# Kernel tuning notes

Measured on AMD Instinct MI355X. Metric: run time of the kernel, lower is better.

The kernel has to match this reference:

```python
import jax, jax.numpy as jnp
import numpy as np

V, C, T, H, L, B = 32000, 1024, 1024, 16, 8, 4
HS = C // H
STD = 0.02


def _layernorm(x, g, b, eps=1e-5):
    m = jnp.mean(x, axis=-1, keepdims=True)
    v = jnp.mean(jnp.square(x - m), axis=-1, keepdims=True)
    return (x - m) * jax.lax.rsqrt(v + eps) * g + b


def setup_inputs() -> dict:
    key = jax.random.key(0)
    ks = jax.random.split(key, 16)
    n = lambda k, shape: (jax.random.normal(k, shape, dtype=jnp.float32) * STD)
    return {
        "index": jax.random.randint(ks[0], (B, T), 0, V),
        "targets": jax.random.randint(ks[1], (B, T), 0, V),
        "tok_emb": n(ks[2], (V, C)),
        "pos_emb": n(ks[3], (T, C)),
        "wq": n(ks[4], (L, C, C)),
        "wk": n(ks[5], (L, C, C)),
        "wv": n(ks[6], (L, C, C)),
        "wo": n(ks[7], (L, C, C)),
        "bo": jnp.zeros((L, C), jnp.float32),
        "w1": n(ks[8], (L, C, 4 * C)),
        "b1": jnp.zeros((L, 4 * C), jnp.float32),
        "w2": n(ks[9], (L, 4 * C, C)),
        "b2": jnp.zeros((L, C), jnp.float32),
        "ln1_g": jnp.ones((L, C), jnp.float32),
        "ln1_b": jnp.zeros((L, C), jnp.float32),
        "ln2_g": jnp.ones((L, C), jnp.float32),
        "ln2_b": jnp.zeros((L, C), jnp.float32),
        "lnf_g": jnp.ones((C,), jnp.float32),
        "lnf_b": jnp.zeros((C,), jnp.float32),
        "lm_w": n(ks[10], (C, V)),
        "lm_b": jnp.zeros((V,), jnp.float32),
    }


def reference(index, targets, tok_emb, pos_emb, wq, wk, wv, wo, bo, w1, b1, w2,
              b2, ln1_g, ln1_b, ln2_g, ln2_b, lnf_g, lnf_b, lm_w, lm_b):
    b, t = index.shape
    x = tok_emb[index] + pos_emb[:t]                      # [B,T,C]
    causal = jnp.tril(jnp.ones((t, t), dtype=bool))       # tril mask
    scale = HS ** -0.5
    for l in range(L):  # fixed small layer loop
        q = (x @ wq[l]).reshape(b, t, H, HS)
        k = (x @ wk[l]).reshape(b, t, H, HS)
        v = (x @ wv[l]).reshape(b, t, H, HS)
        scores = jnp.einsum('bqhd,bkhd->bhqk', q, k) * scale
        scores = jnp.where(causal, scores, -jnp.inf)
        w = jax.nn.softmax(scores, axis=-1)               # dropout p=0 -> identity
        att = jnp.einsum('bhqk,bkhd->bqhd', w, v).reshape(b, t, C)
        x = _layernorm(x + att @ wo[l] + bo[l], ln1_g[l], ln1_b[l])
        h = jax.nn.relu(x @ w1[l] + b1[l])
        x = _layernorm(x + h @ w2[l] + b2[l], ln2_g[l], ln2_b[l])
    x = _layernorm(x, lnf_g, lnf_b)
    logits = (x @ lm_w + lm_b).reshape(b * t, V)
    logp = jax.nn.log_softmax(logits, axis=-1)
    loss = -jnp.take_along_axis(logp, targets.reshape(-1, 1), axis=1).mean()
    return logits, loss
```

## Files before the change

kernel.cpp:

```cpp
#include <hip/hip_runtime.h>

typedef unsigned short u16;
typedef __attribute__((ext_vector_type(4))) float f32x4;
typedef __attribute__((ext_vector_type(8))) short s16x8;
typedef __attribute__((ext_vector_type(4))) short s16x4;

static constexpr int V = 32000;
static constexpr int C = 1024;
static constexpr int T = 1024;
static constexpr int H = 16;
static constexpr int L = 8;
static constexpr int B = 4;
static constexpr int HS = 64;
static constexpr int BT = B * T;
static constexpr int C4 = 4 * C;
static constexpr int C3 = 3 * C;

__device__ __forceinline__ u16 f2bf(float f) {
  union { float f; unsigned u; } v; v.f = f;
  unsigned r = v.u + 0x7fffu + ((v.u >> 16) & 1u);
  return (u16)(r >> 16);
}

__device__ __forceinline__ void gload16(const u16* g, u16* l) {
  __builtin_amdgcn_global_load_lds(
      (const __attribute__((address_space(1))) void*)g,
      (__attribute__((address_space(3))) void*)l, 16, 0, 0);
}

__device__ __forceinline__ float blockReduceSum(float v) {
  __shared__ float red[4];
  int lane = threadIdx.x & 63, w = threadIdx.x >> 6;
#pragma unroll
  for (int m = 32; m >= 1; m >>= 1) v += __shfl_xor(v, m, 64);
  if (lane == 0) red[w] = v;
  __syncthreads();
  float r = red[0] + red[1] + red[2] + red[3];
  __syncthreads();
  return r;
}

__global__ __launch_bounds__(256) void k_embed(
    const int* __restrict__ idx, const float* __restrict__ tok,
    const float* __restrict__ pos, float* __restrict__ x, u16* __restrict__ xb) {
  int bt = blockIdx.x;
  int t = bt & (T - 1);
  int row = idx[bt];
  int tid = threadIdx.x;
  f32x4 tv = ((const f32x4*)(tok + (size_t)row * C))[tid];
  f32x4 pv = ((const f32x4*)(pos + (size_t)t * C))[tid];
  f32x4 y;
  s16x4 yb;
#pragma unroll
  for (int j = 0; j < 4; ++j) {
    y[j] = tv[j] + pv[j];
    yb[j] = (short)f2bf(y[j]);
  }
  ((f32x4*)(x + (size_t)bt * C))[tid] = y;
  ((s16x4*)(xb + (size_t)bt * C))[tid] = yb;
}

__global__ __launch_bounds__(256) void k_transpose(
    const float* __restrict__ W, u16* __restrict__ Wt, int K, int N,
    size_t sW, size_t sWt) {
  __shared__ float tile[64][65];
  const float* Wz = W + sW * blockIdx.z;
  u16* Wtz = Wt + sWt * blockIdx.z;
  int n0 = blockIdx.x * 64, k0 = blockIdx.y * 64;
  int tc = threadIdx.x & 63, tr = threadIdx.x >> 6;
#pragma unroll
  for (int i = 0; i < 16; ++i) {
    int r = tr + i * 4;
    tile[r][tc] = Wz[(size_t)(k0 + r) * N + (n0 + tc)];
  }
  __syncthreads();
#pragma unroll
  for (int i = 0; i < 16; ++i) {
    int r = tr + i * 4;
    Wtz[(size_t)(n0 + r) * K + (k0 + tc)] = f2bf(tile[tc][r]);
  }
}

template <int OUT_BF16, int RELU, int HAS_BIAS, int HAS_RES>
__global__ __launch_bounds__(256, 2) void k_gemm(
    const u16* __restrict__ A, const u16* __restrict__ Bt,
    const float* __restrict__ bias, const float* __restrict__ Res,
    float* __restrict__ Cf, u16* __restrict__ Cb, int M, int N, int K) {
  __shared__ u16 As[3][4096];
  __shared__ u16 Bs[3][4096];
  int tid = threadIdx.x;
  int lane = tid & 63, wid = tid >> 6;
  int lm = lane & 15, lg = lane >> 4;
  int wm = wid >> 1, wn = wid & 1;

  unsigned nbx = gridDim.x;
  unsigned nwg = nbx * gridDim.y;
  unsigned orig = blockIdx.y * nbx + blockIdx.x;
  unsigned f = ((nwg & 7u) == 0u) ? (orig & 7u) * (nwg >> 3) + (orig >> 3) : orig;
  int mb = (int)(f / nbx) * 128, nb = (int)(f % nbx) * 128;

  f32x4 acc[4][4];
#pragma unroll
  for (int i = 0; i < 4; ++i)
#pragma unroll
    for (int j = 0; j < 4; ++j) acc[i][j] = f32x4{0.f, 0.f, 0.f, 0.f};

  int r0 = tid >> 2, q0 = tid & 3;
  int r1 = (256 + tid) >> 2;
  const u16* a0 = A + (size_t)(mb + r0) * K + q0 * 8;
  const u16* a1 = A + (size_t)(mb + r1) * K + q0 * 8;
  const u16* b0 = Bt + (size_t)(nb + r0) * K + q0 * 8;
  const u16* b1 = Bt + (size_t)(nb + r1) * K + q0 * 8;
  const int ld0 = wid * 512, ld1 = 2048 + wid * 512;

  auto stage = [&](int t, int s) {
    int ko = t * 32;
    gload16(a0 + ko, &As[s][ld0]);
    gload16(a1 + ko, &As[s][ld1]);
    gload16(b0 + ko, &Bs[s][ld0]);
    gload16(b1 + ko, &Bs[s][ld1]);
  };

  int nK = K >> 5;
  stage(0, 0);
  stage(1, 1);
  for (int t = 0; t < nK; ++t) {
    int s = t % 3;
    if (t + 1 < nK)
      asm volatile("s_waitcnt vmcnt(4)" ::: "memory");
    else
      asm volatile("s_waitcnt vmcnt(0)" ::: "memory");
    __builtin_amdgcn_s_barrier();
    s16x8 af[4], bfr[4];
#pragma unroll
    for (int m = 0; m < 4; ++m)
      af[m] = *(const s16x8*)&As[s][(wm * 64 + m * 16 + lm) * 32 + lg * 8];
#pragma unroll
    for (int n = 0; n < 4; ++n)
      bfr[n] = *(const s16x8*)&Bs[s][(wn * 64 + n * 16 + lm) * 32 + lg * 8];
    if (t + 2 < nK) stage(t + 2, (t + 2) % 3);
    __builtin_amdgcn_s_setprio(1);
#pragma unroll
    for (int m = 0; m < 4; ++m)
#pragma unroll
      for (int n = 0; n < 4; ++n)
        acc[m][n] = __builtin_amdgcn_mfma_f32_16x16x32_bf16(af[m], bfr[n],
                                                            acc[m][n], 0, 0, 0);
    __builtin_amdgcn_s_setprio(0);
  }
#pragma unroll
  for (int m = 0; m < 4; ++m) {
#pragma unroll
    for (int n = 0; n < 4; ++n) {
      int col = nb + wn * 64 + n * 16 + lm;
      float bv = HAS_BIAS ? bias[col] : 0.0f;
#pragma unroll
      for (int r = 0; r < 4; ++r) {
        int row = mb + wm * 64 + m * 16 + lg * 4 + r;
        float v = acc[m][n][r] + bv;
        if (HAS_RES) v += Res[(size_t)row * N + col];
        if (RELU) v = v > 0.f ? v : 0.f;
        if (OUT_BF16)
          Cb[(size_t)row * N + col] = f2bf(v);
        else
          Cf[(size_t)row * N + col] = v;
      }
    }
  }
}

template <int OUT_BF16, int RELU, int HAS_BIAS, int HAS_RES, int VT>
__global__ __launch_bounds__(512) void k_gemm256(
    const u16* __restrict__ A, const u16* __restrict__ Bt,
    const float* __restrict__ bias, const float* __restrict__ Res,
    float* __restrict__ Cf, u16* __restrict__ Cb, u16* __restrict__ Vtp,
    int M, int N, int K) {
  __shared__ u16 As[2][16384];
  __shared__ u16 Bs[2][16384];
  const int tid = threadIdx.x;
  const int lane = tid & 63, wid = tid >> 6;
  const int lm = lane & 15, lg = lane >> 4;
  const int wr = wid >> 2, wc = wid & 3;

  unsigned nbx = gridDim.x;
  unsigned nwg = nbx * gridDim.y;
  unsigned orig = blockIdx.y * nbx + blockIdx.x;
  unsigned f =
      ((nwg & 7u) == 0u) ? (orig & 7u) * (nwg >> 3) + (orig >> 3) : orig;
  const int mb = (int)(f / nbx) * 256;
  const int nb = (int)(f % nbx) * 256;

  int aoff[4], boff[4], ldso[4];
#pragma unroll
  for (int h = 0; h < 4; ++h) {
    const int kk = h >> 1, p = h & 1;
    int rem = p * 512 + tid;
    int rblk = rem >> 6;
    int rem2 = rem & 63;
    int row16 = rem2 >> 2, psl = rem2 & 3;
    int sl = psl ^ ((row16 >> 1) & 3);
    int grow = rblk * 16 + row16;
    int gk = kk * 32 + sl * 8;
    aoff[h] = (mb + grow) * K + gk;
    boff[h] = (nb + grow) * K + gk;
    ldso[h] = kk * 8192 + p * 4096 + wid * 512;
  }
  const int lo = lm * 32 + ((lg ^ ((lm >> 1) & 3)) << 3);

  f32x4 acc[8][4];
#pragma unroll
  for (int i = 0; i < 8; ++i)
#pragma unroll
    for (int j = 0; j < 4; ++j) acc[i][j] = f32x4{0.f, 0.f, 0.f, 0.f};

  const int nK = K >> 6;
  gload16(A + aoff[0], &As[0][ldso[0]]);
  gload16(A + aoff[1], &As[0][ldso[1]]);
  gload16(Bt + boff[0], &Bs[0][ldso[0]]);
  gload16(Bt + boff[1], &Bs[0][ldso[1]]);
  gload16(A + aoff[2], &As[0][ldso[2]]);
  gload16(A + aoff[3], &As[0][ldso[3]]);
  gload16(Bt + boff[2], &Bs[0][ldso[2]]);
  gload16(Bt + boff[3], &Bs[0][ldso[3]]);
  asm volatile("s_waitcnt vmcnt(4)" ::: "memory");
  __builtin_amdgcn_s_barrier();

  for (int t = 0; t < nK; ++t) {
    const int buf = t & 1, nbuf = buf ^ 1;
    const bool pre = (t + 1 < nK);
    const int nk64 = (t + 1) * 64;
    s16x8 af[4], bfr[4];
#pragma unroll
    for (int m = 0; m < 4; ++m)
      af[m] = *(const s16x8*)&As[buf][(wr * 8 + m) * 512 + lo];
#pragma unroll
    for (int n = 0; n < 4; ++n)
      bfr[n] = *(const s16x8*)&Bs[buf][(wc * 4 + n) * 512 + lo];
    if (pre) {
      gload16(A + aoff[0] + nk64, &As[nbuf][ldso[0]]);
      gload16(A + aoff[1] + nk64, &As[nbuf][ldso[1]]);
    }
    __builtin_amdgcn_s_barrier();
    __builtin_amdgcn_s_setprio(1);
#pragma unroll
    for (int m = 0; m < 4; ++m)
#pragma unroll
      for (int n = 0; n < 4; ++n)
        acc[m][n] = __builtin_amdgcn_mfma_f32_16x16x32_bf16(af[m], bfr[n],
                                                            acc[m][n], 0, 0, 0);
    __builtin_amdgcn_s_setprio(0);
    __builtin_amdgcn_s_barrier();
#pragma unroll
    for (int m = 0; m < 4; ++m)
      af[m] = *(const s16x8*)&As[buf][(wr * 8 + 4 + m) * 512 + lo];
    if (pre) {
      gload16(Bt + boff[0] + nk64, &Bs[nbuf][ldso[0]]);
      gload16(Bt + boff[1] + nk64, &Bs[nbuf][ldso[1]]);
    }
    __builtin_amdgcn_s_barrier();
    __builtin_amdgcn_s_setprio(1);
#pragma unroll
    for (int m = 0; m < 4; ++m)
#pragma unroll
      for (int n = 0; n < 4; ++n)
        acc[m + 4][n] = __builtin_amdgcn_mfma_f32_16x16x32_bf16(
            af[m], bfr[n], acc[m + 4][n], 0, 0, 0);
    __builtin_amdgcn_s_setprio(0);
    __builtin_amdgcn_s_barrier();
#pragma unroll
    for (int m = 0; m < 4; ++m)
      af[m] = *(const s16x8*)&As[buf][8192 + (wr * 8 + m) * 512 + lo];
#pragma unroll
    for (int n = 0; n < 4; ++n)
      bfr[n] = *(const s16x8*)&Bs[buf][8192 + (wc * 4 + n) * 512 + lo];
    if (pre) {
      gload16(A + aoff[2] + nk64, &As[nbuf][ldso[2]]);
      gload16(A + aoff[3] + nk64, &As[nbuf][ldso[3]]);
      asm volatile("s_waitcnt vmcnt(6)" ::: "memory");
    } else {
      asm volatile("s_waitcnt vmcnt(0)" ::: "memory");
    }
    __builtin_amdgcn_s_barrier();
    __builtin_amdgcn_s_setprio(1);
#pragma unroll
    for (int m = 0; m < 4; ++m)
#pragma unroll
      for (int n = 0; n < 4; ++n)
        acc[m][n] = __builtin_amdgcn_mfma_f32_16x16x32_bf16(af[m], bfr[n],
                                                            acc[m][n], 0, 0, 0);
    __builtin_amdgcn_s_setprio(0);
    __builtin_amdgcn_s_barrier();
#pragma unroll
    for (int m = 0; m < 4; ++m)
      af[m] = *(const s16x8*)&As[buf][8192 + (wr * 8 + 4 + m) * 512 + lo];
    if (pre) {
      gload16(Bt + boff[2] + nk64, &Bs[nbuf][ldso[2]]);
      gload16(Bt + boff[3] + nk64, &Bs[nbuf][ldso[3]]);
      asm volatile("s_waitcnt vmcnt(4)" ::: "memory");
    }
    __builtin_amdgcn_s_barrier();
    __builtin_amdgcn_s_setprio(1);
#pragma unroll
    for (int m = 0; m < 4; ++m)
#pragma unroll
      for (int n = 0; n < 4; ++n)
        acc[m + 4][n] = __builtin_amdgcn_mfma_f32_16x16x32_bf16(
            af[m], bfr[n], acc[m + 4][n], 0, 0, 0);
    __builtin_amdgcn_s_setprio(0);
    __builtin_amdgcn_s_barrier();
  }
  if (VT && nb >= 2 * C) {
    int hh = ((nb - 2 * C) >> 6) + wc;
#pragma unroll
    for (int m = 0; m < 8; ++m) {
      int t0 = mb + wr * 128 + m * 16 + lg * 4;
      int bb = t0 >> 10, tt = t0 & (T - 1);
      size_t vbase = ((size_t)(bb * H + hh) * HS) * T + tt;
#pragma unroll
      for (int n = 0; n < 4; ++n) {
        int d = n * 16 + lm;
        s16x4 pk;
#pragma unroll
        for (int r = 0; r < 4; ++r) pk[r] = (short)f2bf(acc[m][n][r]);
        *(s16x4*)&Vtp[vbase + (size_t)d * T] = pk;
      }
    }
    return;
  }
  float bv[4];
#pragma unroll
  for (int n = 0; n < 4; ++n)
    bv[n] = HAS_BIAS ? bias[nb + wc * 64 + n * 16 + lm] : 0.0f;
#pragma unroll
  for (int m = 0; m < 8; ++m) {
#pragma unroll
    for (int r = 0; r < 4; ++r) {
      int row = mb + wr * 128 + m * 16 + lg * 4 + r;
#pragma unroll
      for (int n = 0; n < 4; ++n) {
        int col = nb + wc * 64 + n * 16 + lm;
        float v = acc[m][n][r] + bv[n];
        if (HAS_RES) v += Res[(size_t)row * N + col];
        if (RELU) v = v > 0.f ? v : 0.f;
        if (OUT_BF16)
          Cb[(size_t)row * N + col] = f2bf(v);
        else
          Cf[(size_t)row * N + col] = v;
      }
    }
  }
}

__global__ __launch_bounds__(512) void k_lmhead(
    const u16* __restrict__ A, const u16* __restrict__ Bt,
    const float* __restrict__ bias, float* __restrict__ Cf,
    float* __restrict__ Pp, int M, int N, int K) {
  __shared__ u16 As[3][4096];
  __shared__ u16 Bs[3][8192];
  const int tid = threadIdx.x;
  const int lane = tid & 63, wid = tid >> 6;
  const int lm = lane & 15, lg = lane >> 4;
  const int wr = wid >> 2, wc = wid & 3;

  unsigned nbx = gridDim.x;
  unsigned My = gridDim.y;
  unsigned nwg = nbx * My;
  unsigned orig = blockIdx.y * nbx + blockIdx.x;
  unsigned xcd = orig & 7u, idx = orig >> 3;
  unsigned g = xcd * (nwg >> 3) + idx;
  const int mb = (int)(g % My) * 128;
  const int nb = (int)(g / My) * 256;

  int rr0 = tid & 63;
  int row160 = rr0 >> 2, psl0 = rr0 & 3;
  int sl0 = psl0 ^ ((row160 >> 1) & 3);
  const int aoff = (mb + (tid >> 6) * 16 + row160) * K + sl0 * 8;
  const int lda = wid * 512;
  int boff[2], ldb[2];
#pragma unroll
  for (int p = 0; p < 2; ++p) {
    int rem = p * 512 + tid;
    int rblk = rem >> 6, rr = rem & 63;
    int row16 = rr >> 2, psl = rr & 3;
    int sl = psl ^ ((row16 >> 1) & 3);
    boff[p] = (nb + rblk * 16 + row16) * K + sl * 8;
    ldb[p] = p * 4096 + wid * 512;
  }
  const int lo = lm * 32 + ((lg ^ ((lm >> 1) & 3)) << 3);

  f32x4 acc[4][4];
#pragma unroll
  for (int i = 0; i < 4; ++i)
#pragma unroll
    for (int j = 0; j < 4; ++j) acc[i][j] = f32x4{0.f, 0.f, 0.f, 0.f};

  auto stage = [&](int t, int s) {
    int ko = t * 32;
    gload16(A + aoff + ko, &As[s][lda]);
    gload16(Bt + boff[0] + ko, &Bs[s][ldb[0]]);
    gload16(Bt + boff[1] + ko, &Bs[s][ldb[1]]);
  };

  const int nK = K >> 5;
  stage(0, 0);
  stage(1, 1);
  for (int t = 0; t < nK; ++t) {
    int s = t % 3;
    if (t + 1 < nK)
      asm volatile("s_waitcnt vmcnt(3)" ::: "memory");
    else
      asm volatile("s_waitcnt vmcnt(0)" ::: "memory");
    __builtin_amdgcn_s_barrier();
    s16x8 af[4], bfr[4];
#pragma unroll
    for (int m = 0; m < 4; ++m)
      af[m] = *(const s16x8*)&As[s][(wr * 4 + m) * 512 + lo];
#pragma unroll
    for (int n = 0; n < 4; ++n)
      bfr[n] = *(const s16x8*)&Bs[s][(wc * 4 + n) * 512 + lo];
    if (t + 2 < nK) stage(t + 2, (t + 2) % 3);
    __builtin_amdgcn_s_setprio(1);
#pragma unroll
    for (int m = 0; m < 4; ++m)
#pragma unroll
      for (int n = 0; n < 4; ++n)
        acc[m][n] = __builtin_amdgcn_mfma_f32_16x16x32_bf16(af[m], bfr[n],
                                                            acc[m][n], 0, 0, 0);
    __builtin_amdgcn_s_setprio(0);
  }
  float bv[4];
#pragma unroll
  for (int n = 0; n < 4; ++n) bv[n] = bias[nb + wc * 64 + n * 16 + lm];
#pragma unroll
  for (int m = 0; m < 4; ++m) {
#pragma unroll
    for (int r = 0; r < 4; ++r) {
      int row = mb + wr * 64 + m * 16 + lg * 4 + r;
#pragma unroll
      for (int n = 0; n < 4; ++n) {
        int col = nb + wc * 64 + n * 16 + lm;
        Cf[(size_t)row * N + col] = acc[m][n][r] + bv[n];
      }
    }
  }
  __syncthreads();
  float* redS = (float*)&As[0][0];
  float Sx[4][4];
#pragma unroll
  for (int m = 0; m < 4; ++m)
#pragma unroll
    for (int r = 0; r < 4; ++r)
      Sx[m][r] = __expf(acc[m][0][r] + bv[0]) + __expf(acc[m][1][r] + bv[1]) +
                 __expf(acc[m][2][r] + bv[2]) + __expf(acc[m][3][r] + bv[3]);
#pragma unroll
  for (int d = 1; d < 16; d <<= 1)
#pragma unroll
    for (int m = 0; m < 4; ++m)
#pragma unroll
      for (int r = 0; r < 4; ++r) Sx[m][r] += __shfl_xor(Sx[m][r], d, 16);
  if (lm == 0) {
#pragma unroll
    for (int m = 0; m < 4; ++m)
#pragma unroll
      for (int r = 0; r < 4; ++r)
        redS[(wr * 64 + m * 16 + lg * 4 + r) * 4 + wc] = Sx[m][r];
  }
  __syncthreads();
  if (tid < 128) {
    float srow = redS[tid * 4 + 0] + redS[tid * 4 + 1] + redS[tid * 4 + 2] +
                 redS[tid * 4 + 3];
    Pp[(size_t)(nb >> 8) * M + mb + tid] = srow;
  }
}

__global__ __launch_bounds__(256) void k_attn(
    const u16* __restrict__ qkv, const u16* __restrict__ vt,
    u16* __restrict__ o) {
  constexpr int PP = 72;
  __shared__ u16 Ks[2][64 * 64];
  __shared__ u16 Vs[2][64 * 64];
  __shared__ u16 Ps[4][16 * PP];
  int bid = blockIdx.x;
  int p = bid & 7, h = (bid >> 3) & 15, b = bid >> 7;
  int tid = threadIdx.x, lane = tid & 63, wid = tid >> 6;
  int lm = lane & 15, lg = lane >> 4;
  const size_t rowbase = (size_t)b * T * C3 + (size_t)h * HS;
  const u16* kbase = qkv + rowbase + C;
  const u16* vbase = vt + (size_t)(b * H + h) * HS * T;
  const size_t obase = (size_t)b * T * C + (size_t)h * HS;
  const float scale = 0.125f;
  const int sr = tid >> 3, scs = (tid & 7) ^ (sr & 7);
  const int swz0 = (lg ^ (lm & 7)) * 8;
  const int swz1 = ((4 + lg) ^ (lm & 7)) * 8;

  for (int qi = 0; qi < 2; ++qi) {
    int qt = qi ? (15 - p) : p;
    int qw = qt * 64 + wid * 16;
    s16x8 qf[2];
#pragma unroll
    for (int s = 0; s < 2; ++s)
      qf[s] = *(const s16x8*)&qkv[rowbase + (size_t)(qw + lm) * C3 + s * 32 +
                                  lg * 8];
    float m_[4], l_[4];
    f32x4 oacc[4];
#pragma unroll
    for (int r = 0; r < 4; ++r) { m_[r] = -3e38f; l_[r] = 0.f; }
#pragma unroll
    for (int n = 0; n < 4; ++n) oacc[n] = f32x4{0.f, 0.f, 0.f, 0.f};

    gload16(kbase + (size_t)sr * C3 + scs * 8, &Ks[0][wid * 512]);
    gload16(kbase + (size_t)(sr + 32) * C3 + scs * 8, &Ks[0][2048 + wid * 512]);
    gload16(vbase + (size_t)sr * T + scs * 8, &Vs[0][wid * 512]);
    gload16(vbase + (size_t)(sr + 32) * T + scs * 8, &Vs[0][2048 + wid * 512]);

    for (int kt = 0; kt <= qt; ++kt) {
      int buf = kt & 1;
      bool pre = kt < qt;
      if (pre) {
        int nk = (kt + 1) * 64;
        int nbuf = buf ^ 1;
        gload16(kbase + (size_t)(nk + sr) * C3 + scs * 8, &Ks[nbuf][wid * 512]);
        gload16(kbase + (size_t)(nk + sr + 32) * C3 + scs * 8,
                &Ks[nbuf][2048 + wid * 512]);
        gload16(vbase + (size_t)sr * T + nk + scs * 8, &Vs[nbuf][wid * 512]);
        gload16(vbase + (size_t)(sr + 32) * T + nk + scs * 8,
                &Vs[nbuf][2048 + wid * 512]);
        asm volatile("s_waitcnt vmcnt(4)" ::: "memory");
      } else {
        asm volatile("s_waitcnt vmcnt(0)" ::: "memory");
      }
      __builtin_amdgcn_s_barrier();

      f32x4 s[4];
#pragma unroll
      for (int ch = 0; ch < 4; ++ch) {
        s16x8 k0 = *(const s16x8*)&Ks[buf][(ch * 16 + lm) * 64 + swz0];
        s16x8 k1 = *(const s16x8*)&Ks[buf][(ch * 16 + lm) * 64 + swz1];
        s[ch] = f32x4{0.f, 0.f, 0.f, 0.f};
        s[ch] = __builtin_amdgcn_mfma_f32_16x16x32_bf16(qf[0], k0, s[ch], 0, 0, 0);
        s[ch] = __builtin_amdgcn_mfma_f32_16x16x32_bf16(qf[1], k1, s[ch], 0, 0, 0);
      }
      if (kt == qt) {
#pragma unroll
        for (int ch = 0; ch < 4; ++ch) {
          int col = kt * 64 + ch * 16 + lm;
#pragma unroll
          for (int r = 0; r < 4; ++r) {
            int row = qw + lg * 4 + r;
            s[ch][r] = (col <= row) ? s[ch][r] * scale : -3e38f;
          }
        }
      } else {
#pragma unroll
        for (int ch = 0; ch < 4; ++ch)
#pragma unroll
          for (int r = 0; r < 4; ++r) s[ch][r] *= scale;
      }
      float rmax[4];
#pragma unroll
      for (int r = 0; r < 4; ++r)
        rmax[r] = fmaxf(fmaxf(s[0][r], s[1][r]), fmaxf(s[2][r], s[3][r]));
#pragma unroll
      for (int mm = 1; mm < 16; mm <<= 1)
#pragma unroll
        for (int r = 0; r < 4; ++r)
          rmax[r] = fmaxf(rmax[r], __shfl_xor(rmax[r], mm, 16));
      float alpha[4], rsum[4];
#pragma unroll
      for (int r = 0; r < 4; ++r) {
        float mn = fmaxf(m_[r], rmax[r]);
        alpha[r] = __expf(m_[r] - mn);
        m_[r] = mn;
        rsum[r] = 0.f;
      }
#pragma unroll
      for (int ch = 0; ch < 4; ++ch)
#pragma unroll
        for (int r = 0; r < 4; ++r) {
          float e = __expf(s[ch][r] - m_[r]);
          s[ch][r] = e;
          rsum[r] += e;
        }
#pragma unroll
      for (int mm = 1; mm < 16; mm <<= 1)
#pragma unroll
        for (int r = 0; r < 4; ++r) rsum[r] += __shfl_xor(rsum[r], mm, 16);
#pragma unroll
      for (int r = 0; r < 4; ++r) l_[r] = l_[r] * alpha[r] + rsum[r];
#pragma unroll
      for (int n = 0; n < 4; ++n)
#pragma unroll
        for (int r = 0; r < 4; ++r) oacc[n][r] *= alpha[r];
#pragma unroll
      for (int r = 0; r < 4; ++r) {
        int pr = lg * 4 + r;
#pragma unroll
        for (int ch = 0; ch < 4; ++ch)
          Ps[wid][pr * PP + ch * 16 + lm] = f2bf(s[ch][r]);
      }
      s16x8 pa0 = *(const s16x8*)&Ps[wid][lm * PP + lg * 8];
      s16x8 pa1 = *(const s16x8*)&Ps[wid][lm * PP + 32 + lg * 8];
#pragma unroll
      for (int n = 0; n < 4; ++n) {
        s16x8 v0 = *(const s16x8*)&Vs[buf][(n * 16 + lm) * 64 + swz0];
        s16x8 v1 = *(const s16x8*)&Vs[buf][(n * 16 + lm) * 64 + swz1];
        oacc[n] =
            __builtin_amdgcn_mfma_f32_16x16x32_bf16(pa0, v0, oacc[n], 0, 0, 0);
        oacc[n] =
            __builtin_amdgcn_mfma_f32_16x16x32_bf16(pa1, v1, oacc[n], 0, 0, 0);
      }
      __builtin_amdgcn_s_barrier();
    }
    float inv[4];
#pragma unroll
    for (int r = 0; r < 4; ++r) inv[r] = 1.0f / l_[r];
#pragma unroll
    for (int n = 0; n < 4; ++n)
#pragma unroll
      for (int r = 0; r < 4; ++r)
        o[obase + (size_t)(qw + lg * 4 + r) * C + n * 16 + lm] =
            f2bf(oacc[n][r] * inv[r]);
  }
}

__global__ __launch_bounds__(256) void k_ln(
    const float* __restrict__ in, const float* __restrict__ g,
    const float* __restrict__ bsh, float* __restrict__ xout,
    u16* __restrict__ xbout) {
  int row = blockIdx.x;
  int tid = threadIdx.x;
  f32x4 v = ((const f32x4*)(in + (size_t)row * C))[tid];
  float s = v[0] + v[1] + v[2] + v[3];
  s = blockReduceSum(s);
  float mean = s * (1.0f / C);
  float s2 = 0.f;
#pragma unroll
  for (int j = 0; j < 4; ++j) {
    float d = v[j] - mean;
    s2 += d * d;
  }
  s2 = blockReduceSum(s2);
  float rstd = rsqrtf(s2 * (1.0f / C) + 1e-5f);
  f32x4 gv = ((const f32x4*)g)[tid];
  f32x4 bv = ((const f32x4*)bsh)[tid];
  f32x4 y;
  s16x4 yb;
#pragma unroll
  for (int j = 0; j < 4; ++j) {
    y[j] = (v[j] - mean) * rstd * gv[j] + bv[j];
    yb[j] = (short)f2bf(y[j]);
  }
  ((f32x4*)(xout + (size_t)row * C))[tid] = y;
  ((s16x4*)(xbout + (size_t)row * C))[tid] = yb;
}

__global__ __launch_bounds__(128) void k_rowloss2(
    const float* __restrict__ sums, const float* __restrict__ logits,
    const int* __restrict__ tgt, float* __restrict__ rowloss) {
  int row = blockIdx.x;
  int tid = threadIdx.x;
  float s = (tid < 125) ? sums[(size_t)tid * BT + row] : 0.f;
#pragma unroll
  for (int d = 1; d < 64; d <<= 1) s += __shfl_xor(s, d, 64);
  __shared__ float ss[2];
  if ((tid & 63) == 0) ss[tid >> 6] = s;
  __syncthreads();
  if (tid == 0)
    rowloss[row] = logf(ss[0] + ss[1]) - logits[(size_t)row * V + tgt[row]];
}

__global__ __launch_bounds__(256) void k_lossreduce(
    const float* __restrict__ rowloss, float* __restrict__ out) {
  __shared__ float red[256];
  int tid = threadIdx.x;
  float s = 0.f;
  for (int i = tid; i < BT; i += 256) s += rowloss[i];
  red[tid] = s;
  __syncthreads();
  for (int m = 128; m >= 1; m >>= 1) {
    if (tid < m) red[tid] += red[tid + m];
    __syncthreads();
  }
  if (tid == 0) out[0] = red[0] * (1.0f / BT);
}

extern "C" void kernel_launch(void* const* d_in, const int* in_sizes, int n_in,
                              void* d_out, int out_size, void* d_ws,
                              size_t ws_size, hipStream_t stream) {
  (void)in_sizes; (void)n_in; (void)out_size; (void)ws_size;
  const int* index = (const int*)d_in[0];
  const int* targets = (const int*)d_in[1];
  const float* tok_emb = (const float*)d_in[2];
  const float* pos_emb = (const float*)d_in[3];
  const float* wq = (const float*)d_in[4];
  const float* wk = (const float*)d_in[5];
  const float* wv = (const float*)d_in[6];
  const float* wo = (const float*)d_in[7];
  const float* bo = (const float*)d_in[8];
  const float* w1 = (const float*)d_in[9];
  const float* b1 = (const float*)d_in[10];
  const float* w2 = (const float*)d_in[11];
  const float* b2 = (const float*)d_in[12];
  const float* ln1_g = (const float*)d_in[13];
  const float* ln1_b = (const float*)d_in[14];
  const float* ln2_g = (const float*)d_in[15];
  const float* ln2_b = (const float*)d_in[16];
  const float* lnf_g = (const float*)d_in[17];
  const float* lnf_b = (const float*)d_in[18];
  const float* lm_w = (const float*)d_in[19];
  const float* lm_b = (const float*)d_in[20];

  float* logits = (float*)d_out;
  float* loss = logits + (size_t)BT * V;

  size_t off = 0;
  auto alloc = [&](size_t bytes) -> void* {
    off = (off + 255) & ~(size_t)255;
    void* p = (void*)((char*)d_ws + off);
    off += bytes;
    return p;
  };
  u16* wqkv_t = (u16*)alloc((size_t)L * C3 * C * 2);
  u16* wo_t = (u16*)alloc((size_t)L * C * C * 2);
  u16* w1_t = (u16*)alloc((size_t)L * C * C4 * 2);
  u16* w2_t = (u16*)alloc((size_t)L * C4 * C * 2);
  u16* lmw_t = (u16*)alloc((size_t)V * C * 2);
  float* x = (float*)alloc((size_t)BT * C * 4);
  float* tmp = (float*)alloc((size_t)BT * C * 4);
  u16* xb = (u16*)alloc((size_t)BT * C * 2);
  u16* qkvb = (u16*)alloc((size_t)BT * C3 * 2);
  u16* vtb = (u16*)alloc((size_t)BT * C * 2);
  u16* attb = (u16*)alloc((size_t)BT * C * 2);
  u16* hb = (u16*)alloc((size_t)BT * C4 * 2);
  float* rowloss = (float*)alloc((size_t)BT * 4);
  float* sums = (float*)alloc((size_t)BT * 128 * 4);

  dim3 blk(256);
  dim3 blk5(512);
  k_transpose<<<dim3(C / 64, C / 64, L), blk, 0, stream>>>(
      wq, wqkv_t, C, C, (size_t)C * C, (size_t)C3 * C);
  k_transpose<<<dim3(C / 64, C / 64, L), blk, 0, stream>>>(
      wk, wqkv_t + (size_t)C * C, C, C, (size_t)C * C, (size_t)C3 * C);
  k_transpose<<<dim3(C / 64, C / 64, L), blk, 0, stream>>>(
      wv, wqkv_t + (size_t)2 * C * C, C, C, (size_t)C * C, (size_t)C3 * C);
  k_transpose<<<dim3(C / 64, C / 64, L), blk, 0, stream>>>(
      wo, wo_t, C, C, (size_t)C * C, (size_t)C * C);
  k_transpose<<<dim3(C4 / 64, C / 64, L), blk, 0, stream>>>(
      w1, w1_t, C, C4, (size_t)C * C4, (size_t)C * C4);
  k_transpose<<<dim3(C / 64, C4 / 64, L), blk, 0, stream>>>(
      w2, w2_t, C4, C, (size_t)C4 * C, (size_t)C4 * C);
  k_transpose<<<dim3(V / 64, C / 64, 1), blk, 0, stream>>>(
      lm_w, lmw_t, C, V, 0, 0);

  k_embed<<<BT, blk, 0, stream>>>(index, tok_emb, pos_emb, x, xb);

  dim3 gQKV(C3 / 256, BT / 256);
  dim3 gCC(C / 128, BT / 128);
  dim3 gC4(C4 / 256, BT / 256);
  for (int l = 0; l < L; ++l) {
    const u16* wqkvt = wqkv_t + (size_t)l * C3 * C;
    const u16* wot = wo_t + (size_t)l * C * C;
    const u16* w1t = w1_t + (size_t)l * C * C4;
    const u16* w2t = w2_t + (size_t)l * C4 * C;

    k_gemm256<1, 0, 0, 0, 1><<<gQKV, blk5, 0, stream>>>(
        xb, wqkvt, nullptr, nullptr, nullptr, qkvb, vtb, BT, C3, C);
    k_attn<<<B * H * 8, blk, 0, stream>>>(qkvb, vtb, attb);
    k_gemm<0, 0, 1, 1><<<gCC, blk, 0, stream>>>(
        attb, wot, bo + (size_t)l * C, x, tmp, nullptr, BT, C, C);
    k_ln<<<BT, blk, 0, stream>>>(tmp, ln1_g + (size_t)l * C,
                                 ln1_b + (size_t)l * C, x, xb);
    k_gemm256<1, 1, 1, 0, 0><<<gC4, blk5, 0, stream>>>(
        xb, w1t, b1 + (size_t)l * C4, nullptr, nullptr, hb, nullptr,
        BT, C4, C);
    k_gemm<0, 0, 1, 1><<<gCC, blk, 0, stream>>>(
        hb, w2t, b2 + (size_t)l * C, x, tmp, nullptr, BT, C, C4);
    k_ln<<<BT, blk, 0, stream>>>(tmp, ln2_g + (size_t)l * C,
                                 ln2_b + (size_t)l * C, x, xb);
  }
  k_ln<<<BT, blk, 0, stream>>>(x, lnf_g, lnf_b, x, xb);
  k_lmhead<<<dim3(V / 256, BT / 128), blk5, 0, stream>>>(
      xb, lmw_t, lm_b, logits, sums, BT, V, C);
  k_rowloss2<<<BT, dim3(128), 0, stream>>>(sums, logits, targets, rowloss);
  k_lossreduce<<<1, blk, 0, stream>>>(rowloss, loss);
}
```

Baseline: 2.482 ms.

## Swizzle LDS layout in k_gemm and enlarge lm-head tile to 256x256

The 128x128 GEMM now stores A/B tiles in LDS in 16-row blocks with an XOR swizzle on the 8-element slot, and its fragment reads use the matching swizzled offset. This is meant to reduce LDS bank conflicts. The lm-head kernel moves to 1024-thread blocks with 256x256 tiles, so each block does more reuse of the loaded operands. The cost is larger LDS use and fewer blocks across the GPU. The redS buffer and epilogue indexing must also fit 256 rows and 16 waves, which is not shown and could be a correctness risk.

```diff
diff --git a/kernel.cpp b/kernel.cpp
--- a/kernel.cpp
+++ b/kernel.cpp
@@ -105,13 +105,14 @@
 #pragma unroll
     for (int j = 0; j < 4; ++j) acc[i][j] = f32x4{0.f, 0.f, 0.f, 0.f};
 
-  int r0 = tid >> 2, q0 = tid & 3;
-  int r1 = (256 + tid) >> 2;
-  const u16* a0 = A + (size_t)(mb + r0) * K + q0 * 8;
-  const u16* a1 = A + (size_t)(mb + r1) * K + q0 * 8;
-  const u16* b0 = Bt + (size_t)(nb + r0) * K + q0 * 8;
-  const u16* b1 = Bt + (size_t)(nb + r1) * K + q0 * 8;
+  int row = tid >> 2, psl = tid & 3;
+  int sl = psl ^ (((row & 15) >> 1) & 3);
+  const u16* a0 = A + (size_t)(mb + row) * K + sl * 8;
+  const u16* a1 = A + (size_t)(mb + 64 + row) * K + sl * 8;
+  const u16* b0 = Bt + (size_t)(nb + row) * K + sl * 8;
+  const u16* b1 = Bt + (size_t)(nb + 64 + row) * K + sl * 8;
   const int ld0 = wid * 512, ld1 = 2048 + wid * 512;
+  const int lo = lm * 32 + ((lg ^ ((lm >> 1) & 3)) << 3);
 
   auto stage = [&](int t, int s) {
     int ko = t * 32;
@@ -134,10 +135,10 @@
     s16x8 af[4], bfr[4];
 #pragma unroll
     for (int m = 0; m < 4; ++m)
-      af[m] = *(const s16x8*)&As[s][(wm * 64 + m * 16 + lm) * 32 + lg * 8];
+      af[m] = *(const s16x8*)&As[s][(wm * 4 + m) * 512 + lo];
 #pragma unroll
     for (int n = 0; n < 4; ++n)
-      bfr[n] = *(const s16x8*)&Bs[s][(wn * 64 + n * 16 + lm) * 32 + lg * 8];
+      bfr[n] = *(const s16x8*)&Bs[s][(wn * 4 + n) * 512 + lo];
     if (t + 2 < nK) stage(t + 2, (t + 2) % 3);
     __builtin_amdgcn_s_setprio(1);
 #pragma unroll
@@ -156,14 +157,14 @@
       float bv = HAS_BIAS ? bias[col] : 0.0f;
 #pragma unroll
       for (int r = 0; r < 4; ++r) {
-        int row = mb + wm * 64 + m * 16 + lg * 4 + r;
+        int rw = mb + wm * 64 + m * 16 + lg * 4 + r;
         float v = acc[m][n][r] + bv;
-        if (HAS_RES) v += Res[(size_t)row * N + col];
+        if (HAS_RES) v += Res[(size_t)rw * N + col];
         if (RELU) v = v > 0.f ? v : 0.f;
         if (OUT_BF16)
-          Cb[(size_t)row * N + col] = f2bf(v);
+          Cb[(size_t)rw * N + col] = f2bf(v);
         else
-          Cf[(size_t)row * N + col] = v;
+          Cf[(size_t)rw * N + col] = v;
       }
     }
   }
@@ -351,11 +352,11 @@
   }
 }
 
-__global__ __launch_bounds__(512) void k_lmhead(
+__global__ __launch_bounds__(1024) void k_lmhead(
     const u16* __restrict__ A, const u16* __restrict__ Bt,
     const float* __restrict__ bias, float* __restrict__ Cf,
     float* __restrict__ Pp, int M, int N, int K) {
-  __shared__ u16 As[3][4096];
+  __shared__ u16 As[3][8192];
   __shared__ u16 Bs[3][8192];
   const int tid = threadIdx.x;
   const int lane = tid & 63, wid = tid >> 6;
@@ -368,24 +369,16 @@
   unsigned orig = blockIdx.y * nbx + blockIdx.x;
   unsigned xcd = orig & 7u, idx = orig >> 3;
   unsigned g = xcd * (nwg >> 3) + idx;
-  const int mb = (int)(g % My) * 128;
+  const int mb = (int)(g % My) * 256;
   const int nb = (int)(g / My) * 256;
 
-  int rr0 = tid & 63;
-  int row160 = rr0 >> 2, psl0 = rr0 & 3;
-  int sl0 = psl0 ^ ((row160 >> 1) & 3);
-  const int aoff = (mb + (tid >> 6) * 16 + row160) * K + sl0 * 8;
-  const int lda = wid * 512;
-  int boff[2], ldb[2];
-#pragma unroll
-  for (int p = 0; p < 2; ++p) {
-    int rem = p * 512 + tid;
-    int rblk = rem >> 6, rr = rem & 63;
-    int row16 = rr >> 2, psl = rr & 3;
-    int sl = psl ^ ((row16 >> 1) & 3);
-    boff[p] = (nb + rblk * 16 + row16) * K + sl * 8;
-    ldb[p] = p * 4096 + wid * 512;
-  }
+  int rblk = tid >> 6, rem = tid & 63;
+  int row16 = rem >> 2, psl = rem & 3;
+  int sl = psl ^ ((row16 >> 1) & 3);
+  int grow = rblk * 16 + row16;
+  const int aoff = (mb + grow) * K + sl * 8;
+  const int boff = (nb + grow) * K + sl * 8;
+  const int lds = wid * 512;
   const int lo = lm * 32 + ((lg ^ ((lm >> 1) & 3)) << 3);
 
   f32x4 acc[4][4];
@@ -396,9 +389,8 @@
 
   auto stage = [&](int t, int s) {
     int ko = t * 32;
-    gload16(A + aoff + ko, &As[s][lda]);
-    gload16(Bt + boff[0] + ko, &Bs[s][ldb[0]]);
-    gload16(Bt + boff[1] + ko, &Bs[s][ldb[1]]);
+    gload16(A + aoff + ko, &As[s][lds]);
+    gload16(Bt + boff + ko, &Bs[s][lds]);
   };
 
   const int nK = K >> 5;
@@ -407,7 +399,7 @@
   for (int t = 0; t < nK; ++t) {
     int s = t % 3;
     if (t + 1 < nK)
-      asm volatile("s_waitcnt vmcnt(3)" ::: "memory");
+      asm volatile("s_waitcnt vmcnt(2)" ::: "memory");
     else
       asm volatile("s_waitcnt vmcnt(0)" ::: "memory");
     __builtin_amdgcn_s_barrier();
@@ -466,7 +458,7 @@
         redS[(wr * 64 + m * 16 + lg * 4 + r) * 4 + wc] = Sx[m][r];
   }
   __syncthreads();
-  if (tid < 128) {
+  if (tid < 256) {
     float srow = redS[tid * 4 + 0] + redS[tid * 4 + 1] + redS[tid * 4 + 2] +
                  redS[tid * 4 + 3];
     Pp[(size_t)(nb >> 8) * M + mb + tid] = srow;
@@ -779,7 +771,7 @@
                                  ln2_b + (size_t)l * C, x, xb);
   }
   k_ln<<<BT, blk, 0, stream>>>(x, lnf_g, lnf_b, x, xb);
-  k_lmhead<<<dim3(V / 256, BT / 128), blk5, 0, stream>>>(
+  k_lmhead<<<dim3(V / 256, BT / 256), dim3(1024), 0, stream>>>(
       xb, lmw_t, lm_b, logits, sums, BT, V, C);
   k_rowloss2<<<BT, dim3(128), 0, stream>>>(sums, logits, targets, rowloss);
   k_lossreduce<<<1, blk, 0, stream>>>(rowloss, loss);
```

Result: no change. 2.465 ms (-0.7%).
